# Kernel optimization log

Measured on AMD Instinct MI355X. Metric: run time of the kernel, lower is better.

The kernel has to match this reference:

```python
import jax, jax.numpy as jnp
import numpy as np
import math

D_MODEL = 1024
N_HEADS = 16
HEAD_DIM = D_MODEL // N_HEADS


def get_slopes(n_heads: int) -> jnp.ndarray:
    def pow2_slopes(n):
        start = 2.0 ** (-8.0 / n)
        return np.array([start * start ** i for i in range(n)], dtype=np.float32)
    if math.log2(n_heads).is_integer():
        return jnp.asarray(pow2_slopes(n_heads))
    closest = 2 ** math.floor(math.log2(n_heads))
    base = pow2_slopes(closest)
    extra = pow2_slopes(2 * closest)[::2][: n_heads - closest]
    return jnp.asarray(np.concatenate([base, extra]))


def setup_inputs() -> dict:
    key = jax.random.key(0)
    ks = jax.random.split(key, 9)
    s = 1.0 / math.sqrt(D_MODEL)
    x = jax.random.normal(ks[0], (2, 2048, D_MODEL), dtype=jnp.float32)
    q_w = jax.random.uniform(ks[1], (D_MODEL, D_MODEL), jnp.float32, -s, s)
    q_b = jax.random.uniform(ks[2], (D_MODEL,), jnp.float32, -s, s)
    k_w = jax.random.uniform(ks[3], (D_MODEL, D_MODEL), jnp.float32, -s, s)
    k_b = jax.random.uniform(ks[4], (D_MODEL,), jnp.float32, -s, s)
    v_w = jax.random.uniform(ks[5], (D_MODEL, D_MODEL), jnp.float32, -s, s)
    v_b = jax.random.uniform(ks[6], (D_MODEL,), jnp.float32, -s, s)
    o_w = jax.random.uniform(ks[7], (D_MODEL, D_MODEL), jnp.float32, -s, s)
    o_b = jax.random.uniform(ks[8], (D_MODEL,), jnp.float32, -s, s)
    return {"x": x, "q_w": q_w, "q_b": q_b, "k_w": k_w, "k_b": k_b,
            "v_w": v_w, "v_b": v_b, "o_w": o_w, "o_b": o_b}


def reference(x, q_w, q_b, k_w, k_b, v_w, v_b, o_w, o_b):
    B, S, D = x.shape
    H, hd = N_HEADS, HEAD_DIM
    # torch Linear: y = x @ W.T + b
    Q = (x @ q_w.T + q_b).reshape(B, S, H, hd).transpose(0, 2, 1, 3)  # [B,H,S,hd]
    K = (x @ k_w.T + k_b).reshape(B, S, H, hd).transpose(0, 2, 1, 3)
    V = (x @ v_w.T + v_b).reshape(B, S, H, hd).transpose(0, 2, 1, 3)
    scores = jnp.einsum('bhqd,bhkd->bhqk', Q, K) / math.sqrt(hd)
    # ALiBi bias: slopes[h] * (k_pos - q_pos)
    pos = jnp.arange(S)
    rel = (pos[None, :] - pos[:, None]).astype(scores.dtype)  # [S,S]
    slopes = get_slopes(H)
    scores = scores + slopes[None, :, None, None] * rel[None, None, :, :]
    # causal mask
    causal = pos[None, :] <= pos[:, None]  # [S,S] True where allowed
    scores = jnp.where(causal[None, None], scores, -jnp.inf)
    attn = jax.nn.softmax(scores, axis=-1)  # dropout=0 (eval)
    out = jnp.einsum('bhqk,bhkd->bhqd', attn, V)
    out = out.transpose(0, 2, 1, 3).reshape(B, S, D)
    return out @ o_w.T + o_b
```

## Files before the change

### kernel.cpp

```cpp
#include <hip/hip_runtime.h>

typedef __attribute__((ext_vector_type(8))) short short8;
typedef __attribute__((ext_vector_type(4))) float float4v;
typedef __attribute__((ext_vector_type(4))) short short4v;

#define B_ 2
#define S_ 2048
#define D_ 1024
#define H_ 16
#define HD_ 64
#define M_ 4096
#define LOG2E 1.442695040888963f

__device__ __forceinline__ unsigned short f2bf(float f) {
  unsigned int u = __builtin_bit_cast(unsigned int, f);
  u += 0x7fffu + ((u >> 16) & 1u);
  return (unsigned short)(u >> 16);
}

__device__ __forceinline__ void gload_lds16(const void* g, void* l) {
  __builtin_amdgcn_global_load_lds(
      (const __attribute__((address_space(1))) void*)g,
      (__attribute__((address_space(3))) void*)l, 16, 0, 0);
}

__global__ __launch_bounds__(256, 4) void cvt_kernel(
    const float* __restrict__ x,  const float* __restrict__ qw,
    const float* __restrict__ kw, const float* __restrict__ vw,
    const float* __restrict__ ow, unsigned short* __restrict__ dst)
{
  const int seg = blockIdx.y;
  const float* src;
  size_t doff;
  if (seg < 4)       { src = x + (size_t)seg * 1048576; doff = (size_t)seg * 1048576; }
  else if (seg == 4) { src = qw; doff = 4194304u; }
  else if (seg == 5) { src = kw; doff = 4194304u + 1048576u; }
  else if (seg == 6) { src = vw; doff = 4194304u + 2097152u; }
  else               { src = ow; doff = 4194304u + 3145728u; }
  const size_t i = ((size_t)blockIdx.x * 256 + threadIdx.x) * 4;
  float4v v = *(const float4v*)(src + i);
  short4v p;
#pragma unroll
  for (int r = 0; r < 4; ++r) p[r] = (short)f2bf(v[r]);
  *(short4v*)(dst + doff + i) = p;
}

__global__ __launch_bounds__(256, 2) void gemm_kernel(
    const unsigned short* __restrict__ X,
    const unsigned short* __restrict__ W0, const unsigned short* __restrict__ W1,
    const unsigned short* __restrict__ W2,
    const float* __restrict__ Bi0, const float* __restrict__ Bi1,
    const float* __restrict__ Bi2,
    unsigned short* O0, unsigned short* O1, unsigned short* O2,
    float* OutF, int md0, int md1, int md2)
{
  const int z = blockIdx.z;
  const unsigned short* W  = (z == 0) ? W0  : ((z == 1) ? W1  : W2);
  const float* Bi          = (z == 0) ? Bi0 : ((z == 1) ? Bi1 : Bi2);
  unsigned short* Out      = (z == 0) ? O0  : ((z == 1) ? O1  : O2);
  const int mode           = (z == 0) ? md0 : ((z == 1) ? md1 : md2);

  __shared__ __align__(16) char smem[128 * 32 * 2 * 2];
  char* As = smem;
  char* Bs = smem + 128 * 32 * 2;

  const int t = threadIdx.x, l = t & 63;
  const int w = t >> 6, lr = l & 15, lg = l >> 4;
  const int n0 = blockIdx.x * 128, m0 = blockIdx.y * 128;
  const int wm = (w >> 1) * 64, wn = (w & 1) * 64;

  float4v acc[4][4];
#pragma unroll
  for (int i = 0; i < 4; ++i)
#pragma unroll
    for (int j = 0; j < 4; ++j) acc[i][j] = (float4v){0.f, 0.f, 0.f, 0.f};

  const int c0 = t, c1 = t + 256;
  const int r0 = c0 >> 2, k80 = (c0 & 3) * 8;
  const int r1 = c1 >> 2, k81 = (c1 & 3) * 8;

  for (int k0 = 0; k0 < 1024; k0 += 32) {
    __syncthreads();
    gload_lds16(X + (size_t)(m0 + r0) * 1024 + k0 + k80, As + c0 * 16);
    gload_lds16(X + (size_t)(m0 + r1) * 1024 + k0 + k81, As + c1 * 16);
    gload_lds16(W + (size_t)(n0 + r0) * 1024 + k0 + k80, Bs + c0 * 16);
    gload_lds16(W + (size_t)(n0 + r1) * 1024 + k0 + k81, Bs + c1 * 16);
    __syncthreads();

    short8 af[4], bfr[4];
#pragma unroll
    for (int i = 0; i < 4; ++i)
      af[i] = *(const short8*)(As + (wm + i * 16 + lr) * 64 + lg * 16);
#pragma unroll
    for (int j = 0; j < 4; ++j)
      bfr[j] = *(const short8*)(Bs + (wn + j * 16 + lr) * 64 + lg * 16);
#pragma unroll
    for (int i = 0; i < 4; ++i)
#pragma unroll
      for (int j = 0; j < 4; ++j)
        acc[i][j] = __builtin_amdgcn_mfma_f32_16x16x32_bf16(af[i], bfr[j], acc[i][j], 0, 0, 0);
  }

  float bv[4];
#pragma unroll
  for (int j = 0; j < 4; ++j) bv[j] = Bi[n0 + wn + j * 16 + lr];

#pragma unroll
  for (int i = 0; i < 4; ++i) {
    const int rowb = m0 + wm + i * 16 + lg * 4;
#pragma unroll
    for (int j = 0; j < 4; ++j) {
      const int col = n0 + wn + j * 16 + lr;
      if (mode == 2) {
        const int b = rowb >> 11, s = rowb & 2047;
        const int hh = col >> 6, d = col & 63;
        short4v pk;
#pragma unroll
        for (int r = 0; r < 4; ++r) pk[r] = (short)f2bf(acc[i][j][r] + bv[j]);
        *(short4v*)(Out + ((size_t)(b * H_ + hh) * HD_ + d) * S_ + s) = pk;
      } else if (mode == 1) {
#pragma unroll
        for (int r = 0; r < 4; ++r) {
          const int row = rowb + r;
          const int b = row >> 11, s = row & 2047;
          const int hh = col >> 6, d = col & 63;
          Out[((size_t)(b * H_ + hh) * S_ + s) * HD_ + d] = f2bf(acc[i][j][r] + bv[j]);
        }
      } else {
#pragma unroll
        for (int r = 0; r < 4; ++r)
          OutF[(size_t)(rowb + r) * 1024 + col] = acc[i][j][r] + bv[j];
      }
    }
  }
}

__global__ __launch_bounds__(256, 2) void attn_kernel(
    const unsigned short* __restrict__ Q, const unsigned short* __restrict__ K,
    const unsigned short* __restrict__ VT, unsigned short* __restrict__ O)
{
  __shared__ __align__(16) char smem[32768 + 4 * 4416];

  const int t = threadIdx.x, l = t & 63;
  const int w = t >> 6, lr = l & 15, lg = l >> 4;
  const int bh = blockIdx.x;
  const int it = 31 - (int)blockIdx.y;
  const int h = bh & 15;

  const unsigned short* qbp = Q + (size_t)bh * S_ * HD_;
  const unsigned short* kbp = K + (size_t)bh * S_ * HD_;
  const unsigned short* vbp = VT + (size_t)bh * HD_ * S_;

  const float slope2 = __builtin_amdgcn_exp2f(-0.5f * (float)(h + 1)) * LOG2E;
  const float qksc = 0.125f * LOG2E;

  char* tw = smem + 32768 + w * 4416;

  const int g0 = t, g1 = t + 256;
  const int sr0 = g0 >> 3, sc0 = (g0 & 7) ^ (sr0 & 7);
  const int sr1 = g1 >> 3, sc1 = (g1 & 7) ^ (sr1 & 7);

  const int fchunk = ((4 + lg) ^ (lr & 7)) * 16;
  const int fchunk0 = ((lg) ^ (lr & 7)) * 16;

  const int qrow = it * 64 + w * 16;
  const int qpos = qrow + lr;

  float kb16[4][4];
#pragma unroll
  for (int nj = 0; nj < 4; ++nj)
#pragma unroll
    for (int r = 0; r < 4; ++r)
      kb16[nj][r] = slope2 * (float)(nj * 16 + lg * 4 + r);

  short8 qf[2];
#pragma unroll
  for (int ks = 0; ks < 2; ++ks)
    qf[ks] = *(const short8*)(qbp + (size_t)(qrow + lr) * HD_ + ks * 32 + lg * 8);

  float4v o_acc[4];
#pragma unroll
  for (int dt = 0; dt < 4; ++dt) o_acc[dt] = (float4v){0.f, 0.f, 0.f, 0.f};
  float m_st = -1e30f, l_st = 0.f;

  gload_lds16(kbp + (size_t)sr0 * HD_ + sc0 * 8, smem + g0 * 16);
  gload_lds16(kbp + (size_t)sr1 * HD_ + sc1 * 8, smem + g1 * 16);
  gload_lds16(vbp + (size_t)sr0 * S_ + sc0 * 8, smem + 16384 + g0 * 16);
  gload_lds16(vbp + (size_t)sr1 * S_ + sc1 * 8, smem + 16384 + g1 * 16);
  __syncthreads();

  for (int j = 0; j <= it; ++j) {
    const int cur = j & 1;
    char* Ks = smem + (cur ? 8192 : 0);
    char* Vs = smem + 16384 + (cur ? 8192 : 0);
    if (j < it) {
      char* Kn = smem + (cur ? 0 : 8192);
      char* Vn = smem + 16384 + (cur ? 0 : 8192);
      const int jn = j + 1;
      gload_lds16(kbp + (size_t)(jn * 64 + sr0) * HD_ + sc0 * 8, Kn + g0 * 16);
      gload_lds16(kbp + (size_t)(jn * 64 + sr1) * HD_ + sc1 * 8, Kn + g1 * 16);
      gload_lds16(vbp + (size_t)sr0 * S_ + jn * 64 + sc0 * 8, Vn + g0 * 16);
      gload_lds16(vbp + (size_t)sr1 * S_ + jn * 64 + sc1 * 8, Vn + g1 * 16);
    }

    float4v s_acc[4];
#pragma unroll
    for (int nj = 0; nj < 4; ++nj) {
      s_acc[nj] = (float4v){0.f, 0.f, 0.f, 0.f};
      short8 kf0 = *(const short8*)(Ks + (nj * 16 + lr) * 128 + fchunk0);
      s_acc[nj] = __builtin_amdgcn_mfma_f32_16x16x32_bf16(kf0, qf[0], s_acc[nj], 0, 0, 0);
      short8 kf1 = *(const short8*)(Ks + (nj * 16 + lr) * 128 + fchunk);
      s_acc[nj] = __builtin_amdgcn_mfma_f32_16x16x32_bf16(kf1, qf[1], s_acc[nj], 0, 0, 0);
    }

    const float cj = slope2 * (float)(j * 64);
#pragma unroll
    for (int nj = 0; nj < 4; ++nj)
#pragma unroll
      for (int r = 0; r < 4; ++r)
        s_acc[nj][r] = s_acc[nj][r] * qksc + (cj + kb16[nj][r]);
    if (j == it) {
#pragma unroll
      for (int nj = 0; nj < 4; ++nj)
#pragma unroll
        for (int r = 0; r < 4; ++r) {
          const int kpos = j * 64 + nj * 16 + lg * 4 + r;
          if (kpos > qpos) s_acc[nj][r] = -1e30f;
        }
    }

    float mx = s_acc[0][0];
#pragma unroll
    for (int nj = 0; nj < 4; ++nj)
#pragma unroll
      for (int r = 0; r < 4; ++r) mx = fmaxf(mx, s_acc[nj][r]);
    mx = fmaxf(mx, __shfl_xor(mx, 16, 64));
    mx = fmaxf(mx, __shfl_xor(mx, 32, 64));
    const float mn = fmaxf(m_st, mx);
    const float alpha = __builtin_amdgcn_exp2f(m_st - mn);
    m_st = mn;
    float rsum = 0.f;
#pragma unroll
    for (int nj = 0; nj < 4; ++nj)
#pragma unroll
      for (int r = 0; r < 4; ++r) {
        const float p = __builtin_amdgcn_exp2f(s_acc[nj][r] - mn);
        s_acc[nj][r] = p;
        rsum += p;
      }
    rsum += __shfl_xor(rsum, 16, 64);
    rsum += __shfl_xor(rsum, 32, 64);
    l_st = alpha * l_st + rsum;
#pragma unroll
    for (int dt = 0; dt < 4; ++dt)
#pragma unroll
      for (int r = 0; r < 4; ++r) o_acc[dt][r] *= alpha;

    short8 pT[2];
#pragma unroll
    for (int njp = 0; njp < 2; ++njp)
#pragma unroll
      for (int jj = 0; jj < 4; ++jj) {
        pT[njp][jj]     = (short)f2bf(s_acc[njp * 2][jj]);
        pT[njp][jj + 4] = (short)f2bf(s_acc[njp * 2 + 1][jj]);
      }

    const int vcl = lr & 7;
#pragma unroll
    for (int dt = 0; dt < 4; ++dt) {
      const char* rowp = Vs + (dt * 16 + lr) * 128;
#pragma unroll
      for (int njp = 0; njp < 2; ++njp) {
        const int cA = ((njp * 4 + (lg >> 1)) ^ vcl) * 16 + (lg & 1) * 8;
        const int cB = ((njp * 4 + 2 + (lg >> 1)) ^ vcl) * 16 + (lg & 1) * 8;
        short4v v0 = *(const short4v*)(rowp + cA);
        short4v v1 = *(const short4v*)(rowp + cB);
        short8 vf8;
#pragma unroll
        for (int e = 0; e < 4; ++e) { vf8[e] = v0[e]; vf8[e + 4] = v1[e]; }
        o_acc[dt] = __builtin_amdgcn_mfma_f32_16x16x32_bf16(vf8, pT[njp], o_acc[dt], 0, 0, 0);
      }
    }
    __syncthreads();
  }

#pragma unroll
  for (int dt = 0; dt < 4; ++dt)
#pragma unroll
    for (int r = 0; r < 4; ++r)
      *(float*)(tw + ((dt * 16 + lg * 4 + r) * 17 + lr) * 4) = o_acc[dt][r];
  if (lg == 0) *(float*)(tw + 4352 + lr * 4) = l_st;

  const int q2 = l >> 2, dbase = (l & 3) * 16;
  const float invl = 1.0f / *(const float*)(tw + 4352 + q2 * 4);
  short8 os[2];
#pragma unroll
  for (int i = 0; i < 16; ++i) {
    const float v = *(const float*)(tw + ((dbase + i) * 17 + q2) * 4) * invl;
    os[i >> 3][i & 7] = (short)f2bf(v);
  }
  const int brow = (bh >> 4) * S_;
  unsigned short* op = O + (size_t)(brow + qrow + q2) * 1024 + h * 64 + dbase;
  *(short8*)op = os[0];
  *(short8*)(op + 8) = os[1];
}

extern "C" void kernel_launch(void* const* d_in, const int* in_sizes, int n_in,
                              void* d_out, int out_size, void* d_ws, size_t ws_size,
                              hipStream_t stream) {
  (void)in_sizes; (void)n_in; (void)out_size; (void)ws_size;
  const float* x  = (const float*)d_in[0];
  const float* qw = (const float*)d_in[1];
  const float* qb = (const float*)d_in[2];
  const float* kw = (const float*)d_in[3];
  const float* kb = (const float*)d_in[4];
  const float* vw = (const float*)d_in[5];
  const float* vb = (const float*)d_in[6];
  const float* ow = (const float*)d_in[7];
  const float* ob = (const float*)d_in[8];
  float* out = (float*)d_out;

  unsigned short* xb  = (unsigned short*)d_ws;
  unsigned short* qwb = xb  + (size_t)M_ * D_;
  unsigned short* kwb = qwb + (size_t)D_ * D_;
  unsigned short* vwb = kwb + (size_t)D_ * D_;
  unsigned short* owb = vwb + (size_t)D_ * D_;
  unsigned short* qws = owb + (size_t)D_ * D_;
  unsigned short* kws = qws + (size_t)M_ * D_;
  unsigned short* vws = kws + (size_t)M_ * D_;
  unsigned short* aws = vws + (size_t)M_ * D_;

  cvt_kernel<<<dim3(1024, 8), dim3(256), 0, stream>>>(x, qw, kw, vw, ow, xb);
  gemm_kernel<<<dim3(8, 32, 3), dim3(256), 0, stream>>>(
      xb, qwb, kwb, vwb, qb, kb, vb, qws, kws, vws, out, 1, 1, 2);
  attn_kernel<<<dim3(32, 32), dim3(256), 0, stream>>>(qws, kws, vws, aws);
  gemm_kernel<<<dim3(8, 32, 1), dim3(256), 0, stream>>>(
      aws, owb, owb, owb, ob, ob, ob, aws, aws, aws, out, 0, 0, 0);
}
```

Measured before the change: 193.3 us.

## Stage mode-1 GEMM epilogue through LDS and use packed bf16 conversions

For mode 1 (head-major Q/K layout), the GEMM epilogue now writes the accumulator tile into a padded shared-memory buffer and then has each thread emit contiguous 32-byte bf16 chunks. This replaces scattered 2-byte global stores and is meant to fix the uncoalesced writes. Separately, scalar float-to-bf16 rounding is replaced with the packed two-float conversion intrinsic in the GEMM, in the attention P matrix, and in the attention output. The cost is an extra 16.5KB of LDS per GEMM block, which may lower occupancy, plus added barriers in the epilogue.

After: 196.6 us. About the same (+1.7%).

```diff
diff --git a/kernel.cpp b/kernel.cpp
--- a/kernel.cpp
+++ b/kernel.cpp
@@ -1,8 +1,11 @@
 #include <hip/hip_runtime.h>
+#include <hip/hip_bf16.h>
 
 typedef __attribute__((ext_vector_type(8))) short short8;
 typedef __attribute__((ext_vector_type(4))) float float4v;
 typedef __attribute__((ext_vector_type(4))) short short4v;
+typedef __attribute__((ext_vector_type(4))) unsigned int uint4v;
+typedef __attribute__((ext_vector_type(2))) unsigned int uint2v;
 
 #define B_ 2
 #define S_ 2048
@@ -16,6 +19,13 @@
   unsigned int u = __builtin_bit_cast(unsigned int, f);
   u += 0x7fffu + ((u >> 16) & 1u);
   return (unsigned short)(u >> 16);
+}
+
+__device__ __forceinline__ unsigned int pkbf(float a, float b) {
+  __hip_bfloat162 h = __float22bfloat162_rn(make_float2(a, b));
+  unsigned int u;
+  __builtin_memcpy(&u, &h, sizeof(u));
+  return u;
 }
 
 __device__ __forceinline__ void gload_lds16(const void* g, void* l) {
@@ -61,6 +71,7 @@
   const int mode           = (z == 0) ? md0 : ((z == 1) ? md1 : md2);
 
   __shared__ __align__(16) char smem[128 * 32 * 2 * 2];
+  __shared__ __align__(16) float tb[32 * 132];
   char* As = smem;
   char* Bs = smem + 128 * 32 * 2;
 
@@ -105,31 +116,58 @@
 #pragma unroll
   for (int j = 0; j < 4; ++j) bv[j] = Bi[n0 + wn + j * 16 + lr];
 
-#pragma unroll
-  for (int i = 0; i < 4; ++i) {
-    const int rowb = m0 + wm + i * 16 + lg * 4;
-#pragma unroll
-    for (int j = 0; j < 4; ++j) {
-      const int col = n0 + wn + j * 16 + lr;
-      if (mode == 2) {
-        const int b = rowb >> 11, s = rowb & 2047;
-        const int hh = col >> 6, d = col & 63;
-        short4v pk;
-#pragma unroll
-        for (int r = 0; r < 4; ++r) pk[r] = (short)f2bf(acc[i][j][r] + bv[j]);
-        *(short4v*)(Out + ((size_t)(b * H_ + hh) * HD_ + d) * S_ + s) = pk;
-      } else if (mode == 1) {
-#pragma unroll
-        for (int r = 0; r < 4; ++r) {
-          const int row = rowb + r;
-          const int b = row >> 11, s = row & 2047;
+  if (mode == 1) {
+    const int rbase = (w >> 1) * 16;
+    const int row16 = t >> 3, chunk = t & 7;
+#pragma unroll
+    for (int i = 0; i < 4; ++i) {
+#pragma unroll
+      for (int j = 0; j < 4; ++j)
+#pragma unroll
+        for (int r = 0; r < 4; ++r)
+          tb[(rbase + lg * 4 + r) * 132 + wn + j * 16 + lr] = acc[i][j][r] + bv[j];
+      __syncthreads();
+      const int grow = m0 + ((row16 < 16) ? (i * 16 + row16) : (64 + i * 16 + row16 - 16));
+      const int b = grow >> 11, sl = grow & 2047;
+      const int colg = n0 + chunk * 16;
+      const int hh = colg >> 6, d0 = colg & 63;
+      float4v v4[4];
+#pragma unroll
+      for (int q = 0; q < 4; ++q)
+        v4[q] = *(const float4v*)(tb + row16 * 132 + chunk * 16 + q * 4);
+      uint4v lo, hi;
+#pragma unroll
+      for (int q = 0; q < 2; ++q) {
+        lo[q * 2]     = pkbf(v4[q][0], v4[q][1]);
+        lo[q * 2 + 1] = pkbf(v4[q][2], v4[q][3]);
+        hi[q * 2]     = pkbf(v4[q + 2][0], v4[q + 2][1]);
+        hi[q * 2 + 1] = pkbf(v4[q + 2][2], v4[q + 2][3]);
+      }
+      unsigned short* dst = Out + ((size_t)(b * H_ + hh) * S_ + sl) * HD_ + d0;
+      *(short8*)dst = __builtin_bit_cast(short8, lo);
+      *(short8*)(dst + 8) = __builtin_bit_cast(short8, hi);
+      __syncthreads();
+    }
+  } else {
+#pragma unroll
+    for (int i = 0; i < 4; ++i) {
+      const int rowb = m0 + wm + i * 16 + lg * 4;
+#pragma unroll
+      for (int j = 0; j < 4; ++j) {
+        const int col = n0 + wn + j * 16 + lr;
+        if (mode == 2) {
+          const int b = rowb >> 11, s = rowb & 2047;
           const int hh = col >> 6, d = col & 63;
-          Out[((size_t)(b * H_ + hh) * S_ + s) * HD_ + d] = f2bf(acc[i][j][r] + bv[j]);
+          uint2v pk2;
+          pk2[0] = pkbf(acc[i][j][0] + bv[j], acc[i][j][1] + bv[j]);
+          pk2[1] = pkbf(acc[i][j][2] + bv[j], acc[i][j][3] + bv[j]);
+          *(short4v*)(Out + ((size_t)(b * H_ + hh) * HD_ + d) * S_ + s) =
+              __builtin_bit_cast(short4v, pk2);
+        } else {
+#pragma unroll
+          for (int r = 0; r < 4; ++r)
+            OutF[(size_t)(rowb + r) * 1024 + col] = acc[i][j][r] + bv[j];
         }
-      } else {
-#pragma unroll
-        for (int r = 0; r < 4; ++r)
-          OutF[(size_t)(rowb + r) * 1024 + col] = acc[i][j][r] + bv[j];
       }
     }
   }
@@ -258,12 +296,14 @@
 
     short8 pT[2];
 #pragma unroll
-    for (int njp = 0; njp < 2; ++njp)
-#pragma unroll
-      for (int jj = 0; jj < 4; ++jj) {
-        pT[njp][jj]     = (short)f2bf(s_acc[njp * 2][jj]);
-        pT[njp][jj + 4] = (short)f2bf(s_acc[njp * 2 + 1][jj]);
-      }
+    for (int njp = 0; njp < 2; ++njp) {
+      uint4v u;
+      u[0] = pkbf(s_acc[njp * 2][0], s_acc[njp * 2][1]);
+      u[1] = pkbf(s_acc[njp * 2][2], s_acc[njp * 2][3]);
+      u[2] = pkbf(s_acc[njp * 2 + 1][0], s_acc[njp * 2 + 1][1]);
+      u[3] = pkbf(s_acc[njp * 2 + 1][2], s_acc[njp * 2 + 1][3]);
+      pT[njp] = __builtin_bit_cast(short8, u);
+    }
 
     const int vcl = lr & 7;
 #pragma unroll
@@ -293,16 +333,17 @@
 
   const int q2 = l >> 2, dbase = (l & 3) * 16;
   const float invl = 1.0f / *(const float*)(tw + 4352 + q2 * 4);
-  short8 os[2];
-#pragma unroll
-  for (int i = 0; i < 16; ++i) {
-    const float v = *(const float*)(tw + ((dbase + i) * 17 + q2) * 4) * invl;
-    os[i >> 3][i & 7] = (short)f2bf(v);
+  uint4v os0, os1;
+#pragma unroll
+  for (int k = 0; k < 8; ++k) {
+    const float va = *(const float*)(tw + ((dbase + 2 * k) * 17 + q2) * 4) * invl;
+    const float vb = *(const float*)(tw + ((dbase + 2 * k + 1) * 17 + q2) * 4) * invl;
+    if (k < 4) os0[k] = pkbf(va, vb); else os1[k - 4] = pkbf(va, vb);
   }
   const int brow = (bh >> 4) * S_;
   unsigned short* op = O + (size_t)(brow + qrow + q2) * 1024 + h * 64 + dbase;
-  *(short8*)op = os[0];
-  *(short8*)(op + 8) = os[1];
+  *(short8*)op = __builtin_bit_cast(short8, os0);
+  *(short8*)(op + 8) = __builtin_bit_cast(short8, os1);
 }
 
 extern "C" void kernel_launch(void* const* d_in, const int* in_sizes, int n_in,
```
